# Kernel optimization log

Hardware: AMD Instinct MI355X
Metric: run time of the kernel (lower is better)

The kernel has to match this reference:

```python
import jax, jax.numpy as jnp
import numpy as np

N_NODES = 50000
N_EDGES = 800000
IN_DIM, HIDDEN, OUT_DIM = 256, 128, 64
N_LAYERS = 2
NEG_SLOPE = 0.1


def setup_inputs() -> dict:
    key = jax.random.key(0)
    ks = jax.random.split(key, 10)
    x = jax.random.normal(ks[0], (N_NODES, IN_DIM), dtype=jnp.float32)
    edge_index = jax.random.randint(ks[1], (2, N_EDGES), 0, N_NODES, dtype=jnp.int64)
    s = 1.0 / np.sqrt(IN_DIM)
    enc_W = jax.random.uniform(ks[2], (IN_DIM, HIDDEN), jnp.float32, -s, s)
    enc_b = jax.random.uniform(ks[3], (HIDDEN,), jnp.float32, -s, s)
    sh = 1.0 / np.sqrt(HIDDEN)
    conv_W = jax.random.uniform(ks[4], (N_LAYERS, HIDDEN, HIDDEN), jnp.float32, -sh, sh)
    conv_b = jnp.zeros((N_LAYERS, HIDDEN), dtype=jnp.float32)
    dec_W = jax.random.uniform(ks[5], (HIDDEN, OUT_DIM), jnp.float32, -sh, sh)
    dec_b = jax.random.uniform(ks[6], (OUT_DIM,), jnp.float32, -sh, sh)
    return {"x": x, "edge_index": edge_index, "enc_W": enc_W, "enc_b": enc_b,
            "conv_W": conv_W, "conv_b": conv_b, "dec_W": dec_W, "dec_b": dec_b}


def _gcn_norm(edge_index, num_nodes):
    # PyG gcn_norm with add_self_loops=True, edge_weight=1
    loops = jnp.arange(num_nodes, dtype=edge_index.dtype)
    src = jnp.concatenate([edge_index[0], loops])
    dst = jnp.concatenate([edge_index[1], loops])
    deg = jax.ops.segment_sum(jnp.ones_like(dst, dtype=jnp.float32), dst,
                              num_segments=num_nodes)
    dinv = jnp.where(deg > 0, jax.lax.rsqrt(deg), 0.0)
    norm = dinv[src] * dinv[dst]  # [E+N]
    return src, dst, norm


def _gcn_conv(h, W, b, src, dst, norm, num_nodes):
    h = h @ W                       # [N, H] dense transform (no bias in lin)
    msg = h[src] * norm[:, None]    # gather + scale, [E+N, H]
    out = jax.ops.segment_sum(msg, dst, num_segments=num_nodes)  # scatter-add
    return out + b


def reference(x, edge_index, enc_W, enc_b, conv_W, conv_b, dec_W, dec_b):
    n = x.shape[0]
    src, dst, norm = _gcn_norm(edge_index, n)
    # eval mode: F.dropout(training=False) is identity
    h = jax.nn.leaky_relu(x @ enc_W + enc_b, NEG_SLOPE)
    for i in range(N_LAYERS):
        h = jax.nn.leaky_relu(_gcn_conv(h, conv_W[i], conv_b[i], src, dst, norm, n),
                              NEG_SLOPE)
    return h @ dec_W + dec_b
```

## Files before the change

### kernel.cpp

```cpp
#include <hip/hip_runtime.h>


constexpr int HID = 128;
constexpr float NEG = 0.1f;
constexpr int CAP = 96;
constexpr int FILL_BLKS = 256;

typedef __attribute__((ext_vector_type(8))) short short8;
typedef __attribute__((ext_vector_type(4))) float f32x4;

union frag8 { short8 s; unsigned u[4]; };

__device__ __forceinline__ float lrelu(float v) { return v > 0.f ? v : v * NEG; }

__device__ __forceinline__ unsigned fbits(float f) {
  union { float f; unsigned u; } c; c.f = f; return c.u;
}
__device__ __forceinline__ unsigned short f2bf(float f) {
  unsigned u = fbits(f);
  return (unsigned short)((u + 0x7fffu + ((u >> 16) & 1u)) >> 16);
}
__device__ __forceinline__ float bf2f(unsigned short h) {
  union { unsigned u; float f; } c; c.u = ((unsigned)h) << 16; return c.f;
}

__device__ __forceinline__ void gload16(const unsigned short* g, unsigned short* l) {
  __builtin_amdgcn_global_load_lds((const __attribute__((address_space(1))) unsigned*)g,
                                   (__attribute__((address_space(3))) unsigned*)l, 16, 0, 0);
}

__global__ __launch_bounds__(256) void k_pre(const float* __restrict__ encW,
                                             const float* __restrict__ convW,
                                             const float* __restrict__ decW,
                                             unsigned short* __restrict__ wf_enc,
                                             unsigned short* __restrict__ wf_c0,
                                             unsigned short* __restrict__ wf_c1,
                                             unsigned short* __restrict__ wf_dec,
                                             int* __restrict__ cursor, int N) {
  if (blockIdx.x < 36) {
    int idx = blockIdx.x * 256 + threadIdx.x;
    const float* W; unsigned short* wf; int WN, NT, base;
    if (idx < 4096)      { W = encW;          wf = wf_enc; WN = 128; NT = 8; base = idx; }
    else if (idx < 6144) { W = convW;         wf = wf_c0;  WN = 128; NT = 8; base = idx - 4096; }
    else if (idx < 8192) { W = convW + 16384; wf = wf_c1;  WN = 128; NT = 8; base = idx - 6144; }
    else if (idx < 9216) { W = decW;          wf = wf_dec; WN = 64;  NT = 4; base = idx - 8192; }
    else return;
    int lane = base & 63, tile = base >> 6;
    int nt = tile % NT, ks = tile / NT;
    int col = nt * 16 + (lane & 15);
    int krow = ks * 32 + (lane >> 4) * 8;
    unsigned short* o = wf + (size_t)base * 16;
#pragma unroll
    for (int j = 0; j < 8; ++j) {
      float v = W[(size_t)(krow + j) * WN + col];
      unsigned short hi = f2bf(v);
      o[j] = hi;
      o[8 + j] = f2bf(v - bf2f(hi));
    }
    return;
  }
  int i = (blockIdx.x - 36) * 256 + threadIdx.x;
  if (i < N) cursor[i] = 0;
}

__global__ __launch_bounds__(512) void k_enc_fill(
    const float* __restrict__ A, const unsigned short* __restrict__ wf,
    const float* __restrict__ bias, const int* __restrict__ src,
    const int* __restrict__ dst, int E, int* __restrict__ cursor,
    unsigned short* __restrict__ eidx2, float* __restrict__ h, int M, int encB) {
  __shared__ unsigned short lwf[32768];
  if (blockIdx.x >= encB) {
    for (int e = (blockIdx.x - encB) * 512 + threadIdx.x; e < E;
         e += FILL_BLKS * 512) {
      int d = dst[e];
      int pos = atomicAdd(&cursor[d], 1);
      if (pos < CAP) eidx2[(size_t)d * CAP + pos] = (unsigned short)src[e];
    }
    return;
  }
  constexpr int NT = 8;
  const int wave = threadIdx.x >> 6, lane = threadIdx.x & 63;
  const int q = lane >> 4, c16 = lane & 15;
  const int row0 = blockIdx.x * 128 + wave * 16;
  int r = row0 + c16;
  if (r >= M) r = M - 1;
  const float* ap = A + (size_t)r * 256 + q * 8;
  f32x4 acc[NT];
#pragma unroll
  for (int nt = 0; nt < NT; ++nt) acc[nt] = (f32x4){0.f, 0.f, 0.f, 0.f};
  float av[8];
  *(float4*)&av[0] = *(const float4*)(ap);
  *(float4*)&av[4] = *(const float4*)(ap + 4);
  for (int half = 0; half < 2; ++half) {
    if (half) __syncthreads();
#pragma unroll
    for (int i = 0; i < 8; ++i) {
      int c = wave + i * 8;
      gload16(wf + (size_t)half * 32768 + c * 512 + lane * 8, lwf + c * 512);
    }
    asm volatile("s_waitcnt vmcnt(0)" ::: "memory");
    __syncthreads();
    for (int ksl = 0; ksl < 4; ++ksl) {
      frag8 ahi, alo;
      float res[8];
#pragma unroll
      for (int i = 0; i < 8; ++i) {
        union { unsigned u; float f; } t; t.u = fbits(av[i]) & 0xffff0000u;
        res[i] = av[i] - t.f;
      }
#pragma unroll
      for (int j = 0; j < 4; ++j) {
        ahi.u[j] = __builtin_amdgcn_perm(fbits(av[2 * j + 1]), fbits(av[2 * j]),
                                         0x07060302u);
        alo.u[j] = __builtin_amdgcn_perm(fbits(res[2 * j + 1]), fbits(res[2 * j]),
                                         0x07060302u);
      }
      int ks = half * 4 + ksl;
      if (ks + 1 < 8) {
        *(float4*)&av[0] = *(const float4*)(ap + (ks + 1) * 32);
        *(float4*)&av[4] = *(const float4*)(ap + (ks + 1) * 32 + 4);
      }
      const unsigned short* wp = lwf + ksl * NT * 1024 + lane * 16;
#pragma unroll
      for (int nt = 0; nt < NT; ++nt) {
        short8 bhi = *(const short8*)(wp);
        short8 blo = *(const short8*)(wp + 8);
        acc[nt] = __builtin_amdgcn_mfma_f32_16x16x32_bf16(ahi.s, bhi, acc[nt], 0, 0, 0);
        acc[nt] = __builtin_amdgcn_mfma_f32_16x16x32_bf16(ahi.s, blo, acc[nt], 0, 0, 0);
        acc[nt] = __builtin_amdgcn_mfma_f32_16x16x32_bf16(alo.s, bhi, acc[nt], 0, 0, 0);
        wp += 1024;
      }
    }
  }
  float bv[NT];
#pragma unroll
  for (int nt = 0; nt < NT; ++nt) bv[nt] = bias[nt * 16 + c16];
#pragma unroll
  for (int rr = 0; rr < 4; ++rr) {
    int gr = row0 + q * 4 + rr;
    if (gr >= M) continue;
#pragma unroll
    for (int nt = 0; nt < NT; ++nt)
      h[(size_t)gr * 128 + nt * 16 + c16] = lrelu(acc[nt][rr] + bv[nt]);
  }
}

template <int NT, int KS, int MODE>
__global__ __launch_bounds__(512) void k_mfma(const float* __restrict__ A,
                                              const unsigned short* __restrict__ wf,
                                              const float* __restrict__ bias,
                                              const int* __restrict__ deg,
                                              void* __restrict__ Cout, int M) {
  constexpr int K = KS * 32;
  constexpr int NOUT = NT * 16;
  constexpr int CH = KS * NT * 2;
  __shared__ unsigned short lwf[KS * NT * 1024];
  const int wave = threadIdx.x >> 6, lane = threadIdx.x & 63;
  const int q = lane >> 4, c16 = lane & 15;
  const int row0 = blockIdx.x * 128 + wave * 16;
  int r = row0 + c16;
  if (r >= M) r = M - 1;
  const float* ap = A + (size_t)r * K + q * 8;
  f32x4 acc[NT];
#pragma unroll
  for (int nt = 0; nt < NT; ++nt) acc[nt] = (f32x4){0.f, 0.f, 0.f, 0.f};
  float av[8];
  *(float4*)&av[0] = *(const float4*)(ap);
  *(float4*)&av[4] = *(const float4*)(ap + 4);
#pragma unroll
  for (int i = 0; i < CH / 8; ++i) {
    int c = wave + i * 8;
    gload16(wf + c * 512 + lane * 8, lwf + c * 512);
  }
  asm volatile("s_waitcnt vmcnt(0)" ::: "memory");
  __syncthreads();
  for (int ks = 0; ks < KS; ++ks) {
    frag8 ahi, alo;
    float res[8];
#pragma unroll
    for (int i = 0; i < 8; ++i) {
      union { unsigned u; float f; } t; t.u = fbits(av[i]) & 0xffff0000u;
      res[i] = av[i] - t.f;
    }
#pragma unroll
    for (int j = 0; j < 4; ++j) {
      ahi.u[j] = __builtin_amdgcn_perm(fbits(av[2 * j + 1]), fbits(av[2 * j]),
                                       0x07060302u);
      alo.u[j] = __builtin_amdgcn_perm(fbits(res[2 * j + 1]), fbits(res[2 * j]),
                                       0x07060302u);
    }
    if (ks + 1 < KS) {
      *(float4*)&av[0] = *(const float4*)(ap + (ks + 1) * 32);
      *(float4*)&av[4] = *(const float4*)(ap + (ks + 1) * 32 + 4);
    }
    const unsigned short* wp = lwf + ks * NT * 1024 + lane * 16;
#pragma unroll
    for (int nt = 0; nt < NT; ++nt) {
      short8 bhi = *(const short8*)(wp);
      short8 blo = *(const short8*)(wp + 8);
      acc[nt] = __builtin_amdgcn_mfma_f32_16x16x32_bf16(ahi.s, bhi, acc[nt], 0, 0, 0);
      acc[nt] = __builtin_amdgcn_mfma_f32_16x16x32_bf16(ahi.s, blo, acc[nt], 0, 0, 0);
      acc[nt] = __builtin_amdgcn_mfma_f32_16x16x32_bf16(alo.s, bhi, acc[nt], 0, 0, 0);
      wp += 1024;
    }
  }
  float bv[NT];
  if (MODE == 2) {
#pragma unroll
    for (int nt = 0; nt < NT; ++nt) bv[nt] = bias[nt * 16 + c16];
  }
#pragma unroll
  for (int rr = 0; rr < 4; ++rr) {
    int gr = row0 + q * 4 + rr;
    if (gr >= M) continue;
    if (MODE == 1) {
      float dv = rsqrtf((float)deg[gr] + 1.0f);
#pragma unroll
      for (int nt = 0; nt < NT; ++nt)
        ((unsigned short*)Cout)[(size_t)gr * NOUT + nt * 16 + c16] =
            f2bf(acc[nt][rr] * dv);
    } else {
#pragma unroll
      for (int nt = 0; nt < NT; ++nt)
        ((float*)Cout)[(size_t)gr * NOUT + nt * 16 + c16] = acc[nt][rr] + bv[nt];
    }
  }
}

__global__ __launch_bounds__(256) void k_gather(const int* __restrict__ deg,
                                                const unsigned short* __restrict__ eidx2,
                                                const unsigned short* __restrict__ t,
                                                const float* __restrict__ bias,
                                                float* __restrict__ h, int N) {
  int node = (blockIdx.x * 256 + threadIdx.x) >> 4;
  int lane = threadIdx.x & 15;
  if (node >= N) return;
  const uint4* t4 = (const uint4*)t;
  int dtrue = deg[node];
  int d = dtrue > CAP ? CAP : dtrue;
  const unsigned short* ep = eidx2 + (size_t)node * CAP;
  float acc[8] = {};
#define ADDV(v)                                         \
  {                                                     \
    unsigned dw[4] = {(v).x, (v).y, (v).z, (v).w};      \
    _Pragma("unroll") for (int i = 0; i < 4; ++i) {     \
      union { unsigned u; float f; } lo, hi;            \
      lo.u = dw[i] << 16;                               \
      hi.u = dw[i] & 0xffff0000u;                       \
      acc[2 * i] += lo.f;                               \
      acc[2 * i + 1] += hi.f;                           \
    }                                                   \
  }
  {
    uint4 vs = t4[(size_t)node * 16 + lane];
    ADDV(vs);
  }
  int e = 0;
  for (; e + 8 <= d; e += 8) {
    int4 sa = *(const int4*)(ep + e);
    unsigned s0 = (unsigned)sa.x & 0xffffu, s1 = (unsigned)sa.x >> 16;
    unsigned s2 = (unsigned)sa.y & 0xffffu, s3 = (unsigned)sa.y >> 16;
    unsigned s4 = (unsigned)sa.z & 0xffffu, s5 = (unsigned)sa.z >> 16;
    unsigned s6 = (unsigned)sa.w & 0xffffu, s7 = (unsigned)sa.w >> 16;
    uint4 v0 = t4[(size_t)s0 * 16 + lane];
    uint4 v1 = t4[(size_t)s1 * 16 + lane];
    uint4 v2 = t4[(size_t)s2 * 16 + lane];
    uint4 v3 = t4[(size_t)s3 * 16 + lane];
    uint4 v4 = t4[(size_t)s4 * 16 + lane];
    uint4 v5 = t4[(size_t)s5 * 16 + lane];
    uint4 v6 = t4[(size_t)s6 * 16 + lane];
    uint4 v7 = t4[(size_t)s7 * 16 + lane];
    ADDV(v0); ADDV(v1); ADDV(v2); ADDV(v3);
    ADDV(v4); ADDV(v5); ADDV(v6); ADDV(v7);
  }
  for (; e < d; ++e) {
    unsigned s = ep[e];
    uint4 v = t4[(size_t)s * 16 + lane];
    ADDV(v);
  }
#undef ADDV
  float w = rsqrtf((float)dtrue + 1.0f);
  float* hp = h + (size_t)node * HID + lane * 8;
  const float* bp = bias + lane * 8;
  float4 o1, o2;
  float* o = (float*)&o1;
#pragma unroll
  for (int i = 0; i < 4; ++i) o[i] = lrelu(acc[i] * w + bp[i]);
  o = (float*)&o2;
#pragma unroll
  for (int i = 0; i < 4; ++i) o[i] = lrelu(acc[4 + i] * w + bp[4 + i]);
  *(float4*)hp = o1;
  *(float4*)(hp + 4) = o2;
}

extern "C" void kernel_launch(void* const* d_in, const int* in_sizes, int n_in,
                              void* d_out, int out_size, void* d_ws, size_t ws_size,
                              hipStream_t stream) {
  const float* x = (const float*)d_in[0];
  const int* ei = (const int*)d_in[1];
  const float* enc_W = (const float*)d_in[2];
  const float* enc_b = (const float*)d_in[3];
  const float* conv_W = (const float*)d_in[4];
  const float* conv_b = (const float*)d_in[5];
  const float* dec_W = (const float*)d_in[6];
  const float* dec_b = (const float*)d_in[7];
  float* out = (float*)d_out;

  const int IN_DIM = 256;
  const int N = in_sizes[0] / IN_DIM;
  const int E = in_sizes[1] / 2;
  const int* src = ei;
  const int* dst = ei + E;

  char* wp = (char*)d_ws;
  auto alloc = [&](size_t bytes) {
    void* p = wp;
    wp += (bytes + 255) & ~(size_t)255;
    return p;
  };
  int* cursor = (int*)alloc((size_t)N * 4);
  unsigned short* eidx2 = (unsigned short*)alloc((size_t)N * CAP * 2);
  float* h = (float*)alloc((size_t)N * HID * 4);
  unsigned short* t = (unsigned short*)alloc((size_t)N * HID * 2);
  unsigned short* wf_enc = (unsigned short*)alloc((size_t)8 * 8 * 64 * 16 * 2);
  unsigned short* wf_c0 = (unsigned short*)alloc((size_t)4 * 8 * 64 * 16 * 2);
  unsigned short* wf_c1 = (unsigned short*)alloc((size_t)4 * 8 * 64 * 16 * 2);
  unsigned short* wf_dec = (unsigned short*)alloc((size_t)4 * 4 * 64 * 16 * 2);

  k_pre<<<36 + (N + 255) / 256, 256, 0, stream>>>(enc_W, conv_W, dec_W, wf_enc, wf_c0,
                                                  wf_c1, wf_dec, cursor, N);

  const int encB = (N + 127) / 128;
  k_enc_fill<<<encB + FILL_BLKS, 512, 0, stream>>>(x, wf_enc, enc_b, src, dst, E,
                                                   cursor, eidx2, h, N, encB);

  const int gm = (N + 127) / 128;
  for (int l = 0; l < 2; ++l) {
    const unsigned short* wf = l ? wf_c1 : wf_c0;
    k_mfma<8, 4, 1><<<gm, 512, 0, stream>>>(h, wf, nullptr, cursor, t, N);
    k_gather<<<(N * 16 + 255) / 256, 256, 0, stream>>>(
        cursor, eidx2, t, conv_b + (size_t)l * HID, h, N);
  }

  k_mfma<4, 4, 2><<<gm, 512, 0, stream>>>(h, wf_dec, dec_b, nullptr, out, N);
}
```

Measured before the change: 247.2 us.

## Pad degree counters, partition fill by destination range, split weight hi/lo planes

```diff
diff --git a/kernel.cpp b/kernel.cpp
--- a/kernel.cpp
+++ b/kernel.cpp
@@ -5,6 +5,7 @@
 constexpr float NEG = 0.1f;
 constexpr int CAP = 96;
 constexpr int FILL_BLKS = 256;
+constexpr int CSTR = 8;
 
 typedef __attribute__((ext_vector_type(8))) short short8;
 typedef __attribute__((ext_vector_type(4))) float f32x4;
@@ -39,28 +40,29 @@
                                              int* __restrict__ cursor, int N) {
   if (blockIdx.x < 36) {
     int idx = blockIdx.x * 256 + threadIdx.x;
-    const float* W; unsigned short* wf; int WN, NT, base;
-    if (idx < 4096)      { W = encW;          wf = wf_enc; WN = 128; NT = 8; base = idx; }
-    else if (idx < 6144) { W = convW;         wf = wf_c0;  WN = 128; NT = 8; base = idx - 4096; }
-    else if (idx < 8192) { W = convW + 16384; wf = wf_c1;  WN = 128; NT = 8; base = idx - 6144; }
-    else if (idx < 9216) { W = decW;          wf = wf_dec; WN = 64;  NT = 4; base = idx - 8192; }
+    const float* W; unsigned short* wf; int WN, NT, base, PL;
+    if (idx < 4096)      { W = encW;          wf = wf_enc; WN = 128; NT = 8; base = idx;        PL = 32768; }
+    else if (idx < 6144) { W = convW;         wf = wf_c0;  WN = 128; NT = 8; base = idx - 4096; PL = 16384; }
+    else if (idx < 8192) { W = convW + 16384; wf = wf_c1;  WN = 128; NT = 8; base = idx - 6144; PL = 16384; }
+    else if (idx < 9216) { W = decW;          wf = wf_dec; WN = 64;  NT = 4; base = idx - 8192; PL = 8192; }
     else return;
     int lane = base & 63, tile = base >> 6;
     int nt = tile % NT, ks = tile / NT;
     int col = nt * 16 + (lane & 15);
     int krow = ks * 32 + (lane >> 4) * 8;
-    unsigned short* o = wf + (size_t)base * 16;
+    unsigned short* ohi = wf + (size_t)base * 8;
+    unsigned short* olo = ohi + PL;
 #pragma unroll
     for (int j = 0; j < 8; ++j) {
       float v = W[(size_t)(krow + j) * WN + col];
       unsigned short hi = f2bf(v);
-      o[j] = hi;
-      o[8 + j] = f2bf(v - bf2f(hi));
+      ohi[j] = hi;
+      olo[j] = f2bf(v - bf2f(hi));
     }
     return;
   }
   int i = (blockIdx.x - 36) * 256 + threadIdx.x;
-  if (i < N) cursor[i] = 0;
+  if (i < N) cursor[i * CSTR] = 0;
 }
 
 __global__ __launch_bounds__(512) void k_enc_fill(
@@ -70,11 +72,16 @@
     unsigned short* __restrict__ eidx2, float* __restrict__ h, int M, int encB) {
   __shared__ unsigned short lwf[32768];
   if (blockIdx.x >= encB) {
-    for (int e = (blockIdx.x - encB) * 512 + threadIdx.x; e < E;
-         e += FILL_BLKS * 512) {
+    int g = blockIdx.x & 7;
+    int rk = (blockIdx.x - encB) >> 3;
+    int lo = (int)(((long long)g * M) >> 3);
+    int hi = (int)(((long long)(g + 1) * M) >> 3);
+    for (int e = rk * 512 + threadIdx.x; e < E; e += 32 * 512) {
       int d = dst[e];
-      int pos = atomicAdd(&cursor[d], 1);
-      if (pos < CAP) eidx2[(size_t)d * CAP + pos] = (unsigned short)src[e];
+      if (d >= lo && d < hi) {
+        int pos = atomicAdd(&cursor[d * CSTR], 1);
+        if (pos < CAP) eidx2[(size_t)d * CAP + pos] = (unsigned short)src[e];
+      }
     }
     return;
   }
@@ -96,7 +103,10 @@
 #pragma unroll
     for (int i = 0; i < 8; ++i) {
       int c = wave + i * 8;
-      gload16(wf + (size_t)half * 32768 + c * 512 + lane * 8, lwf + c * 512);
+      const unsigned short* s = (c < 32)
+          ? wf + half * 16384 + c * 512
+          : wf + 32768 + half * 16384 + (c - 32) * 512;
+      gload16(s + lane * 8, lwf + c * 512);
     }
     asm volatile("s_waitcnt vmcnt(0)" ::: "memory");
     __syncthreads();
@@ -120,15 +130,15 @@
         *(float4*)&av[0] = *(const float4*)(ap + (ks + 1) * 32);
         *(float4*)&av[4] = *(const float4*)(ap + (ks + 1) * 32 + 4);
       }
-      const unsigned short* wp = lwf + ksl * NT * 1024 + lane * 16;
+      const unsigned short* wph = lwf + ksl * NT * 512 + lane * 8;
 #pragma unroll
       for (int nt = 0; nt < NT; ++nt) {
-        short8 bhi = *(const short8*)(wp);
-        short8 blo = *(const short8*)(wp + 8);
+        short8 bhi = *(const short8*)(wph);
+        short8 blo = *(const short8*)(wph + 16384);
         acc[nt] = __builtin_amdgcn_mfma_f32_16x16x32_bf16(ahi.s, bhi, acc[nt], 0, 0, 0);
         acc[nt] = __builtin_amdgcn_mfma_f32_16x16x32_bf16(ahi.s, blo, acc[nt], 0, 0, 0);
         acc[nt] = __builtin_amdgcn_mfma_f32_16x16x32_bf16(alo.s, bhi, acc[nt], 0, 0, 0);
-        wp += 1024;
+        wph += 512;
       }
     }
   }
@@ -153,8 +163,9 @@
                                               void* __restrict__ Cout, int M) {
   constexpr int K = KS * 32;
   constexpr int NOUT = NT * 16;
+  constexpr int PL = KS * NT * 512;
   constexpr int CH = KS * NT * 2;
-  __shared__ unsigned short lwf[KS * NT * 1024];
+  __shared__ unsigned short lwf[2 * PL];
   const int wave = threadIdx.x >> 6, lane = threadIdx.x & 63;
   const int q = lane >> 4, c16 = lane & 15;
   const int row0 = blockIdx.x * 128 + wave * 16;
@@ -193,15 +204,15 @@
       *(float4*)&av[0] = *(const float4*)(ap + (ks + 1) * 32);
       *(float4*)&av[4] = *(const float4*)(ap + (ks + 1) * 32 + 4);
     }
-    const unsigned short* wp = lwf + ks * NT * 1024 + lane * 16;
+    const unsigned short* wph = lwf + ks * NT * 512 + lane * 8;
 #pragma unroll
     for (int nt = 0; nt < NT; ++nt) {
-      short8 bhi = *(const short8*)(wp);
-      short8 blo = *(const short8*)(wp + 8);
+      short8 bhi = *(const short8*)(wph);
+      short8 blo = *(const short8*)(wph + PL);
       acc[nt] = __builtin_amdgcn_mfma_f32_16x16x32_bf16(ahi.s, bhi, acc[nt], 0, 0, 0);
       acc[nt] = __builtin_amdgcn_mfma_f32_16x16x32_bf16(ahi.s, blo, acc[nt], 0, 0, 0);
       acc[nt] = __builtin_amdgcn_mfma_f32_16x16x32_bf16(alo.s, bhi, acc[nt], 0, 0, 0);
-      wp += 1024;
+      wph += 512;
     }
   }
   float bv[NT];
@@ -214,7 +225,7 @@
     int gr = row0 + q * 4 + rr;
     if (gr >= M) continue;
     if (MODE == 1) {
-      float dv = rsqrtf((float)deg[gr] + 1.0f);
+      float dv = rsqrtf((float)deg[gr * CSTR] + 1.0f);
 #pragma unroll
       for (int nt = 0; nt < NT; ++nt)
         ((unsigned short*)Cout)[(size_t)gr * NOUT + nt * 16 + c16] =
@@ -236,7 +247,7 @@
   int lane = threadIdx.x & 15;
   if (node >= N) return;
   const uint4* t4 = (const uint4*)t;
-  int dtrue = deg[node];
+  int dtrue = deg[node * CSTR];
   int d = dtrue > CAP ? CAP : dtrue;
   const unsigned short* ep = eidx2 + (size_t)node * CAP;
   float acc[8] = {};
@@ -318,7 +329,7 @@
     wp += (bytes + 255) & ~(size_t)255;
     return p;
   };
-  int* cursor = (int*)alloc((size_t)N * 4);
+  int* cursor = (int*)alloc((size_t)N * CSTR * 4);
   unsigned short* eidx2 = (unsigned short*)alloc((size_t)N * CAP * 2);
   float* h = (float*)alloc((size_t)N * HID * 4);
   unsigned short* t = (unsigned short*)alloc((size_t)N * HID * 2);
```

Result: slower. 264.7 us (+7.1%).
